# Optimization experiments

Measured on AMD Instinct MI355X. Metric: run time of the kernel, lower is better.

The kernel has to match this reference:

```python
import jax, jax.numpy as jnp
import numpy as np

D_MODEL, D_STATE, D_CONV, EXPAND = 768, 16, 4, 2
D_INNER = EXPAND * D_MODEL        # 1536
DT_RANK = (D_MODEL + 15) // 16    # 48
B, L = 4, 1024
LN_EPS = 1e-5


def _causal_dw_conv(x, w, b):
    # x: [b,l,d], w: [d,k], b: [d] -- depthwise causal conv along l
    k = w.shape[1]
    xp = jnp.pad(x, ((0, 0), (k - 1, 0), (0, 0)))
    out = jnp.zeros_like(x)
    for i in range(k):  # k = 4, tiny fixed loop
        out = out + xp[:, i:i + x.shape[1], :] * w[:, i]
    return out + b


def _selective_scan(u, delta, A, Bm, Cm, Dp):
    # u, delta: [b,l,d]; A: [d,n]; Bm, Cm: [b,l,n]; Dp: [d]
    def step(h, inp):
        d_t, B_t, C_t, u_t = inp                         # [b,d],[b,n],[b,n],[b,d]
        dA = jnp.exp(d_t[:, :, None] * A)                # [b,d,n]
        h = dA * h + (d_t * u_t)[:, :, None] * B_t[:, None, :]
        return h, jnp.einsum('bdn,bn->bd', h, C_t)
    b, l, d = u.shape
    h0 = jnp.zeros((b, d, A.shape[1]), u.dtype)
    xs = (jnp.swapaxes(delta, 0, 1), jnp.swapaxes(Bm, 0, 1),
          jnp.swapaxes(Cm, 0, 1), jnp.swapaxes(u, 0, 1))
    _, ys = jax.lax.scan(step, h0, xs)                   # ys: [l,b,d]
    return jnp.swapaxes(ys, 0, 1) + u * Dp


def _mamba_dir(xz, conv_w, conv_bias, xp_w, dtp_w, dtp_bias, A_log, Dp):
    x, z = jnp.split(xz, 2, axis=-1)                     # each [b,l,d_inner]
    x = jax.nn.silu(_causal_dw_conv(x, conv_w, conv_bias))
    x_dbl = x @ xp_w.T                                   # [b,l,R+2N]
    dt, Bm, Cm = jnp.split(x_dbl, [DT_RANK, DT_RANK + D_STATE], axis=-1)
    dt = jax.nn.softplus(dt @ dtp_w.T + dtp_bias)        # [b,l,d_inner]
    A = -jnp.exp(A_log)                                  # [d_inner,n]
    y = _selective_scan(x, dt, A, Bm, Cm, Dp)
    return y * jax.nn.silu(z)


def _block_single(h, ln_w, ln_b, in_w, conv_w, conv_bias, xp_w, dtp_w, dtp_bias,
                  A_log, D_p, conv_w_b, conv_bias_b, xp_w_b, dtp_w_b, dtp_bias_b,
                  A_b_log, D_b, out_w):
    # LayerNorm
    mu = jnp.mean(h, -1, keepdims=True)
    var = jnp.mean(jnp.square(h - mu), -1, keepdims=True)
    hn = (h - mu) * jax.lax.rsqrt(var + LN_EPS) * ln_w + ln_b
    # Mamba (bimamba v2): shared in_proj/out_proj, fwd + flipped bwd scan
    xz = hn @ in_w.T                                     # [b,l,2*d_inner]
    out_f = _mamba_dir(xz, conv_w, conv_bias, xp_w, dtp_w, dtp_bias, A_log, D_p)
    out_b = _mamba_dir(xz[:, ::-1], conv_w_b, conv_bias_b, xp_w_b, dtp_w_b,
                       dtp_bias_b, A_b_log, D_b)
    return (out_f + out_b[:, ::-1]) @ out_w.T            # [b,l,d_model]


def setup_inputs() -> dict:
    key = jax.random.key(0)
    ks = iter(jax.random.split(key, 40))
    f = lambda *s: jax.random.normal(next(ks), s, jnp.float32)
    p = {}
    p['h_r'] = f(B, L, D_MODEL)
    p['h_i'] = f(B, L, D_MODEL)
    # leading axis 2 = (real-branch mamba_r, imag-branch mamba_i) parameters
    p['ln_w'] = jnp.ones((2, D_MODEL), jnp.float32)
    p['ln_b'] = jnp.zeros((2, D_MODEL), jnp.float32)
    p['in_w'] = f(2, 2 * D_INNER, D_MODEL) * 0.02
    a_init = jnp.broadcast_to(jnp.log(jnp.arange(1, D_STATE + 1, dtype=jnp.float32)),
                              (2, D_INNER, D_STATE))
    for pre in ('', 'b_'):
        sfx = '_b' if pre else ''
        p['conv_w' + sfx] = f(2, D_INNER, D_CONV) * 0.2
        p['conv_bias' + sfx] = f(2, D_INNER) * 0.02
        p['xp_w' + sfx] = f(2, DT_RANK + 2 * D_STATE, D_INNER) * 0.02
        p['dtp_w' + sfx] = f(2, D_INNER, DT_RANK) * 0.1
        p['dtp_bias' + sfx] = f(2, D_INNER) * 0.5
        p['A_log' + sfx if not pre else 'A_b_log'] = a_init
        p['D_p' + sfx if not pre else 'D_b'] = f(2, D_INNER) * 0.1
    p['out_w'] = f(2, D_MODEL, D_INNER) * 0.02
    return p


def reference(h_r, h_i, ln_w, ln_b, in_w, conv_w, conv_bias, xp_w, dtp_w,
              dtp_bias, A_log, D_p, conv_w_b, conv_bias_b, xp_w_b, dtp_w_b,
              dtp_bias_b, A_b_log, D_b, out_w):
    h = jnp.stack([h_r, h_i])                            # [2,b,l,d_model]
    out = jax.vmap(_block_single)(h, ln_w, ln_b, in_w, conv_w, conv_bias, xp_w,
                                  dtp_w, dtp_bias, A_log, D_p, conv_w_b,
                                  conv_bias_b, xp_w_b, dtp_w_b, dtp_bias_b,
                                  A_b_log, D_b, out_w)
    return (out[0], out[1])
```

## Files before the change

### kernel.cpp

```cpp
#include <hip/hip_runtime.h>
#include <hip/hip_bf16.h>
#include <math.h>


#define BB 4
#define LL 1024
#define DM 768
#define DI 1536
#define RK 48
#define NS 16
#define CH 32
#define CLEN 32
#define DB6 (DI / 256)
#define XSPLIT 4
#define XKC2 (DI / XSPLIT)

typedef __attribute__((ext_vector_type(8))) short bf16x8;
typedef __attribute__((ext_vector_type(4))) float f32x4;
typedef unsigned short us;
typedef unsigned int uns;

__device__ __forceinline__ float siluf(float x) {
    return x / (1.f + __expf(-x));
}
__device__ __forceinline__ float softplusf(float x) {
    return fmaxf(x, 0.f) + __logf(1.f + __expf(-fabsf(x)));
}
__device__ __forceinline__ us f2bf(float x) {
    __hip_bfloat16 h = __float2bfloat16(x);
    return *(us*)&h;
}
__device__ __forceinline__ float bf2f(uns v) {
    uns u = v << 16;
    return *(float*)&u;
}
__device__ __forceinline__ unsigned pack2bf(float a, float b) {
    return (unsigned)f2bf(a) | ((unsigned)f2bf(b) << 16);
}
__device__ __forceinline__ void async_cp16(const void* g, void* l) {
    __builtin_amdgcn_global_load_lds(
        (const __attribute__((address_space(1))) void*)g,
        (__attribute__((address_space(3))) void*)l, 16, 0, 0);
}
__device__ __forceinline__ float pow8(float e1, float* p) {
    float e2 = e1 * e1, e4 = e2 * e2, e8 = e4 * e4;
    p[0] = e1;      p[1] = e2;      p[2] = e2 * e1; p[3] = e4;
    p[4] = e4 * e1; p[5] = e4 * e2; p[6] = e4 * p[2]; p[7] = e8;
    return e8;
}

__global__ __launch_bounds__(256)
void zero_kernel(float4* __restrict__ p, int n4)
{
    int i = blockIdx.x * 256 + threadIdx.x;
    if (i < n4) p[i] = (float4){0.f, 0.f, 0.f, 0.f};
}

__global__ __launch_bounds__(256)
void ln_kernel(const float* __restrict__ h, const float* __restrict__ w,
               const float* __restrict__ bvec, us* __restrict__ out)
{
    int row = blockIdx.x;
    const float* x = h + (size_t)row * DM;
    int tid = threadIdx.x;
    float v[3];
    float s = 0.f, s2 = 0.f;
#pragma unroll
    for (int j = 0; j < 3; ++j) {
        v[j] = x[tid + j * 256];
        s += v[j];
        s2 += v[j] * v[j];
    }
#pragma unroll
    for (int off = 32; off > 0; off >>= 1) {
        s += __shfl_down(s, off);
        s2 += __shfl_down(s2, off);
    }
    __shared__ float sw[4], sw2[4], stat[2];
    int wid = tid >> 6;
    if ((tid & 63) == 0) { sw[wid] = s; sw2[wid] = s2; }
    __syncthreads();
    if (tid == 0) {
        float a = sw[0] + sw[1] + sw[2] + sw[3];
        float a2 = sw2[0] + sw2[1] + sw2[2] + sw2[3];
        float mu = a * (1.f / DM);
        float var = a2 * (1.f / DM) - mu * mu;
// ... 2 lines not shown
    }
    __syncthreads();
    float mu = stat[0], rs = stat[1];
    us* o = out + (size_t)row * DM;
#pragma unroll
    for (int j = 0; j < 3; ++j) {
        int i = tid + j * 256;
        o[i] = f2bf((v[j] - mu) * rs * w[i] + bvec[i]);
    }
}

__global__ __launch_bounds__(256)
void cast_kernel(const float* __restrict__ x, us* __restrict__ y)
{
    int i = (blockIdx.x * 256 + threadIdx.x) * 4;
    float4 v = *(const float4*)(x + i);
    y[i + 0] = f2bf(v.x);
    y[i + 1] = f2bf(v.y);
    y[i + 2] = f2bf(v.z);
    y[i + 3] = f2bf(v.w);
}

__global__ __launch_bounds__(256)
void gemm_mfma_bt(const us* __restrict__ A, int lda,
                  const us* __restrict__ B, int ldb,
                  us* __restrict__ C, int ldc, int K)
{
    __shared__ us As[128 * 32];
    __shared__ us Bs[128 * 32];
    int tid = threadIdx.x;
    int wave = tid >> 6, lane = tid & 63;
    int wm = wave & 1, wn = wave >> 1;
    int quad = lane >> 4, lr = lane & 15;
    int m0 = blockIdx.y * 128, n0 = blockIdx.x * 128;

    f32x4 acc[4][4];
#pragma unroll
    for (int i = 0; i < 4; ++i)
#pragma unroll
        for (int j = 0; j < 4; ++j) acc[i][j] = (f32x4){0.f, 0.f, 0.f, 0.f};

    for (int kt = 0; kt < K; kt += 32) {
#pragma unroll
        for (int i = 0; i < 2; ++i) {
            int idx = tid + i * 256;
            int row = idx >> 2, col = (idx & 3) * 8;
            async_cp16(A + (size_t)(m0 + row) * lda + kt + col, &As[idx * 8]);
            async_cp16(B + (size_t)(n0 + row) * ldb + kt + col, &Bs[idx * 8]);
        }
        __syncthreads();

        bf16x8 af[4], bf[4];
#pragma unroll
        for (int mt = 0; mt < 4; ++mt)
            af[mt] = *(const bf16x8*)(&As[(wm * 64 + mt * 16 + lr) * 32 + quad * 8]);
#pragma unroll
        for (int nt = 0; nt < 4; ++nt)
            bf[nt] = *(const bf16x8*)(&Bs[(wn * 64 + nt * 16 + lr) * 32 + quad * 8]);
#pragma unroll
        for (int mt = 0; mt < 4; ++mt)
#pragma unroll
            for (int nt = 0; nt < 4; ++nt)
                acc[mt][nt] = __builtin_amdgcn_mfma_f32_16x16x32_bf16(
                    af[mt], bf[nt], acc[mt][nt], 0, 0, 0);
        __syncthreads();
    }

#pragma unroll
    for (int mt = 0; mt < 4; ++mt)
#pragma unroll
        for (int nt = 0; nt < 4; ++nt)
#pragma unroll
            for (int e = 0; e < 4; ++e) {
                int m = m0 + wm * 64 + mt * 16 + quad * 4 + e;
                int n = n0 + wn * 64 + nt * 16 + lr;
                C[(size_t)m * ldc + n] = f2bf(acc[mt][nt][e]);
            }
}

__global__ __launch_bounds__(256)
void gemm_mfma_bt64(const us* __restrict__ A, int lda,
                    const us* __restrict__ B, int ldb,
                    float* __restrict__ C, int ldc, int K)
{
    __shared__ us As[64 * 32];
    __shared__ us Bs[128 * 32];
    int tid = threadIdx.x;
    int wave = tid >> 6, lane = tid & 63;
    int wm = wave & 1, wn = wave >> 1;
    int quad = lane >> 4, lr = lane & 15;
    int m0 = blockIdx.y * 64, n0 = blockIdx.x * 128;

    f32x4 acc[2][4];
#pragma unroll
    for (int i = 0; i < 2; ++i)
#pragma unroll
        for (int j = 0; j < 4; ++j) acc[i][j] = (f32x4){0.f, 0.f, 0.f, 0.f};

    for (int kt = 0; kt < K; kt += 32) {
        {
            int row = tid >> 2, col = (tid & 3) * 8;
            async_cp16(A + (size_t)(m0 + row) * lda + kt + col, &As[tid * 8]);
        }
#pragma unroll
        for (int i = 0; i < 2; ++i) {
            int idx = tid + i * 256;
            int row = idx >> 2, col = (idx & 3) * 8;
            async_cp16(B + (size_t)(n0 + row) * ldb + kt + col, &Bs[idx * 8]);
        }
        __syncthreads();

        bf16x8 af[2], bf[4];
#pragma unroll
        for (int mt = 0; mt < 2; ++mt)
            af[mt] = *(const bf16x8*)(&As[(wm * 32 + mt * 16 + lr) * 32 + quad * 8]);
#pragma unroll
        for (int nt = 0; nt < 4; ++nt)
            bf[nt] = *(const bf16x8*)(&Bs[(wn * 64 + nt * 16 + lr) * 32 + quad * 8]);
#pragma unroll
        for (int mt = 0; mt < 2; ++mt)
#pragma unroll
            for (int nt = 0; nt < 4; ++nt)
                acc[mt][nt] = __builtin_amdgcn_mfma_f32_16x16x32_bf16(
                    af[mt], bf[nt], acc[mt][nt], 0, 0, 0);
        __syncthreads();
    }

#pragma unroll
    for (int mt = 0; mt < 2; ++mt)
#pragma unroll
        for (int nt = 0; nt < 4; ++nt)
#pragma unroll
            for (int e = 0; e < 4; ++e) {
                int m = m0 + wm * 32 + mt * 16 + quad * 4 + e;
                int n = n0 + wn * 64 + nt * 16 + lr;
                C[(size_t)m * ldc + n] = acc[mt][nt][e];
            }
}

#define CT 32
#define CD 64
__device__ __forceinline__ float4 dw4(float4 x0, float4 x1, float4 x2, float4 x3,
                                      float4 wa, float4 wb, float4 wc, float4 wd,
                                      float4 cb)
{
    float4 o;
    o.x = cb.x + x0.x * wa.x + x1.x * wa.y + x2.x * wa.z + x3.x * wa.w;
    o.y = cb.y + x0.y * wb.x + x1.y * wb.y + x2.y * wb.z + x3.y * wb.w;
    o.z = cb.z + x0.z * wc.x + x1.z * wc.y + x2.z * wc.z + x3.z * wc.w;
    o.w = cb.w + x0.w * wd.x + x1.w * wd.y + x2.w * wd.z + x3.w * wd.w;
    return o;
}

__global__ __launch_bounds__(256)
void conv_fused(const us* __restrict__ xz,
                const float* __restrict__ wf, const float* __restrict__ cbf,
                const float* __restrict__ wb, const float* __restrict__ cbb,
                us* __restrict__ xcf16, us* __restrict__ xcb16)
{
    int d0 = blockIdx.x * CD;
    int s0 = blockIdx.y * CT;
    int b  = blockIdx.z;
    int tid = threadIdx.x;

    __shared__ float XT[CT + 6][CD + 4];

    for (int i = tid; i < (CT + 6) * (CD / 4); i += 256) {
        int r = i >> 4;
        int c4 = i & 15;
        int s = s0 - 3 + r;
        float4 v = (float4){0.f, 0.f, 0.f, 0.f};
        if (s >= 0 && s < LL) {
            uint2 w = *(const uint2*)(xz + ((size_t)(b * LL + s)) * (2 * DI)
                                      + d0 + c4 * 4);
            v.x = bf2f(w.x & 0xffffu); v.y = bf2f(w.x >> 16);
            v.z = bf2f(w.y & 0xffffu); v.w = bf2f(w.y >> 16);
        }
        *(float4*)(&XT[r][c4 * 4]) = v;
    }

    int d4 = tid & 15;
    int sr = tid >> 4;
    int d = d0 + d4 * 4;
    float4 wf0 = *(const float4*)(wf + (size_t)(d + 0) * 4);
    float4 wf1 = *(const float4*)(wf + (size_t)(d + 1) * 4);
    float4 wf2 = *(const float4*)(wf + (size_t)(d + 2) * 4);
    float4 wf3 = *(const float4*)(wf + (size_t)(d + 3) * 4);
    float4 wb0 = *(const float4*)(wb + (size_t)(d + 0) * 4);
    float4 wb1 = *(const float4*)(wb + (size_t)(d + 1) * 4);
    float4 wb2 = *(const float4*)(wb + (size_t)(d + 2) * 4);
    float4 wb3 = *(const float4*)(wb + (size_t)(d + 3) * 4);
    float4 cf  = *(const float4*)(cbf + d);
    float4 cbv = *(const float4*)(cbb + d);
    __syncthreads();

    float4 x4[8];
// ... 2 lines not shown
        x4[j] = *(const float4*)(&XT[2 * sr + j][d4 * 4]);

#pragma unroll
    for (int q = 0; q < 2; ++q) {
        int s = s0 + 2 * sr + q;
        float4 of = dw4(x4[q + 0], x4[q + 1], x4[q + 2], x4[q + 3],
                        wf0, wf1, wf2, wf3, cf);
        of.x = siluf(of.x); of.y = siluf(of.y);
        of.z = siluf(of.z); of.w = siluf(of.w);
        size_t fi = ((size_t)(b * LL + s)) * DI + d;
        uint2 pf; pf.x = pack2bf(of.x, of.y); pf.y = pack2bf(of.z, of.w);
        *(uint2*)(&xcf16[fi]) = pf;
        float4 ob = dw4(x4[q + 6], x4[q + 5], x4[q + 4], x4[q + 3],
                        wb0, wb1, wb2, wb3, cbv);
        ob.x = siluf(ob.x); ob.y = siluf(ob.y);
        ob.z = siluf(ob.z); ob.w = siluf(ob.w);
        size_t bi = ((size_t)(b * LL + (LL - 1 - s))) * DI + d;
        uint2 pb; pb.x = pack2bf(ob.x, ob.y); pb.y = pack2bf(ob.z, ob.w);
        *(uint2*)(&xcb16[bi]) = pb;
    }
}

__global__ __launch_bounds__(256)
void xproj_mfma(const us* __restrict__ a0, const us* __restrict__ a1,
                const us* __restrict__ w0, const us* __restrict__ w1,
                float* __restrict__ xd0, float* __restrict__ xd1)
{
    int z = blockIdx.z;
    const us* A = z ? a1 : a0;
    const us* W = z ? w1 : w0;
    float* out = z ? xd1 : xd0;

    __shared__ us As[64 * 32];
    __shared__ us Ws[80 * 32];
    int tid = threadIdx.x;
    int wave = tid >> 6, lane = tid & 63;
    int quad = lane >> 4, lr = lane & 15;
    int m0 = blockIdx.y * 64;
    int k0 = blockIdx.x * XKC2;

    f32x4 acc[5];
#pragma unroll
    for (int j = 0; j < 5; ++j) acc[j] = (f32x4){0.f, 0.f, 0.f, 0.f};

    for (int kt = 0; kt < XKC2; kt += 32) {
        {
            int row = tid >> 2, col = (tid & 3) * 8;
            async_cp16(A + (size_t)(m0 + row) * DI + k0 + kt + col, &As[tid * 8]);
        }
        {
            int row = tid >> 2, col = (tid & 3) * 8;
            async_cp16(W + (size_t)row * DI + k0 + kt + col, &Ws[tid * 8]);
        }
        if (tid < 64) {
// ... 3 lines not shown
        }
        __syncthreads();

        bf16x8 af = *(const bf16x8*)(&As[(wave * 16 + lr) * 32 + quad * 8]);
#pragma unroll
        for (int j = 0; j < 5; ++j) {
            bf16x8 bf = *(const bf16x8*)(&Ws[(j * 16 + lr) * 32 + quad * 8]);
            acc[j] = __builtin_amdgcn_mfma_f32_16x16x32_bf16(af, bf, acc[j], 0, 0, 0);
        }
        __syncthreads();
    }

#pragma unroll
    for (int j = 0; j < 5; ++j)
#pragma unroll
        for (int e = 0; e < 4; ++e) {
            int m = m0 + wave * 16 + quad * 4 + e;
            int n = j * 16 + lr;
            atomicAdd(&out[(size_t)m * 80 + n], acc[j][e]);
        }
}

__global__ __launch_bounds__(256)
void dtproj2(const float* __restrict__ xd0, const float* __restrict__ xd1,
             const float* __restrict__ W0, const float* __restrict__ W1,
             const float* __restrict__ b0, const float* __restrict__ b1,
             const us* __restrict__ u0, const us* __restrict__ u1,
             uns* __restrict__ si0, uns* __restrict__ si1)
{
    int z = blockIdx.z;
    const float* A = z ? xd1 : xd0;
    const float* W = z ? W1 : W0;
    const float* bias = z ? b1 : b0;
    const us* U = z ? u1 : u0;
    uns* SI = z ? si1 : si0;

    __shared__ float As[48][132];
    __shared__ float Ws[48][68];
    int tid = threadIdx.x;
    int m0 = blockIdx.y * 128, n0 = blockIdx.x * 64;

    for (int i = tid; i < 1536; i += 256) {
        int r = i / 12, kg = i % 12;
        float4 v = *(const float4*)(A + (size_t)(m0 + r) * 80 + kg * 4);
        As[kg * 4 + 0][r] = v.x; As[kg * 4 + 1][r] = v.y;
        As[kg * 4 + 2][r] = v.z; As[kg * 4 + 3][r] = v.w;
    }
    for (int i = tid; i < 768; i += 256) {
        int r = i / 12, kg = i % 12;
        float4 u = *(const float4*)(W + (size_t)(n0 + r) * RK + kg * 4);
        Ws[kg * 4 + 0][r] = u.x; Ws[kg * 4 + 1][r] = u.y;
        Ws[kg * 4 + 2][r] = u.z; Ws[kg * 4 + 3][r] = u.w;
    }
    __syncthreads();

    int tx = tid & 15, ty = tid >> 4;
    float acc[8][4];
#pragma unroll
// ... 35 lines not shown
        s.w = (uns)f2bf(o.w) | (up.y & 0xffff0000u);
        *(uint4*)(SI + off) = s;
    }
}

__device__ __forceinline__ bool a_is_canonical8(const float* Alog, int d, int half)
{
    bool ok = true;
    const float4* a4 = (const float4*)(Alog + (size_t)d * NS + half * 8);
#pragma unroll
    for (int j = 0; j < 2; ++j) {
        float4 v = a4[j];
        float b0 = (float)(half * 8 + 4 * j + 1), b1 = (float)(half * 8 + 4 * j + 2);
        float b2 = (float)(half * 8 + 4 * j + 3), b3 = (float)(half * 8 + 4 * j + 4);
        ok = ok && (fabsf(__expf(v.x) - b0) < 1e-3f * b0)
                && (fabsf(__expf(v.y) - b1) < 1e-3f * b1)
                && (fabsf(__expf(v.z) - b2) < 1e-3f * b2)
                && (fabsf(__expf(v.w) - b3) < 1e-3f * b3);
    }
    return ok;
}

__global__ __launch_bounds__(512)
void scan_p1_b(const uns* __restrict__ si0, const uns* __restrict__ si1,
               const float* __restrict__ xd0, const float* __restrict__ xd1,
               const float* __restrict__ al0, const float* __restrict__ al1,
               uns* __restrict__ PQ0g, uns* __restrict__ PQ1g)
{
    int z = blockIdx.z;
    const uns* SI = z ? si1 : si0;
    const float* xdbl = z ? xd1 : xd0;
    const float* Alog = z ? al1 : al0;
    uns* PQ = z ? PQ1g : PQ0g;

    int c = blockIdx.y;
    int b = blockIdx.x / DB6;
    int dblk = (blockIdx.x % DB6) * 256;
    int tid = threadIdx.x;
    int dl = tid >> 1, half = tid & 1;
    int d = dblk + dl;
    int wave = tid >> 6, lane = tid & 63;

    bool afast = a_is_canonical8(Alog, d, half);

    __shared__ float Bs[CLEN * NS];
    __shared__ uns DU[2][8][256];
    for (int i = tid; i < CLEN * NS; i += 512) {
        int t = i >> 4, n = i & 15;
        Bs[i] = xdbl[((size_t)(b * LL + c * CLEN + t)) * 80 + 48 + n];
    }

    size_t rowbase = ((size_t)b * LL + c * CLEN) * DI + dblk;
#define STAGE_S(s, dbuf)                                                   \
    async_cp16(SI + rowbase + (size_t)((s) * 8 + wave) * DI + lane * 4,    \
               &DU[dbuf][wave][lane * 4]);

    STAGE_S(0, 0);

    float q[8];
#pragma unroll
    for (int n = 0; n < 8; ++n) q[n] = 0.f;
    float dtsum = 0.f;

    if (afast) {
#pragma unroll
        for (int s = 0; s < 4; ++s) {
            __syncthreads();
            if (s < 3) STAGE_S(s + 1, (s + 1) & 1);
            int buf = s & 1;
#pragma unroll
            for (int t8 = 0; t8 < 8; ++t8) {
                uns pk = DU[buf][t8][dl];
                float dtv = bf2f(pk & 0xffffu), uv = bf2f(pk >> 16);
                float du = dtv * uv;
                dtsum += dtv;
                float dA[8];
                float e8 = pow8(__expf(-dtv), dA);
                float sc = half ? e8 : 1.f;
                const float4* b4 = (const float4*)(Bs + (s * 8 + t8) * NS + half * 8);
                float4 B0 = b4[0], B1 = b4[1];
                q[0] = (dA[0] * sc) * q[0] + du * B0.x;
                q[1] = (dA[1] * sc) * q[1] + du * B0.y;
                q[2] = (dA[2] * sc) * q[2] + du * B0.z;
                q[3] = (dA[3] * sc) * q[3] + du * B0.w;
                q[4] = (dA[4] * sc) * q[4] + du * B1.x;
                q[5] = (dA[5] * sc) * q[5] + du * B1.y;
                q[6] = (dA[6] * sc) * q[6] + du * B1.z;
                q[7] = (dA[7] * sc) * q[7] + du * B1.w;
            }
        }
        float P[8];
        float e8 = pow8(__expf(-dtsum), P);
        float sc = half ? e8 : 1.f;
        uns* o = PQ + (size_t)c * (BB * DI * NS) + (size_t)(b * DI + d) * NS
               + half * 8;
        uint4 s0, s1;
        s0.x = pack2bf(P[0] * sc, q[0]); s0.y = pack2bf(P[1] * sc, q[1]);
        s0.z = pack2bf(P[2] * sc, q[2]); s0.w = pack2bf(P[3] * sc, q[3]);
        s1.x = pack2bf(P[4] * sc, q[4]); s1.y = pack2bf(P[5] * sc, q[5]);
        s1.z = pack2bf(P[6] * sc, q[6]); s1.w = pack2bf(P[7] * sc, q[7]);
        *(uint4*)(o) = s0;
        *(uint4*)(o + 4) = s1;
    } else {
        float Av[8];
        {
            const float4* a4 = (const float4*)(Alog + (size_t)d * NS + half * 8);
#pragma unroll
            for (int j = 0; j < 2; ++j) {
                float4 v = a4[j];
                Av[4 * j + 0] = -__expf(v.x); Av[4 * j + 1] = -__expf(v.y);
                Av[4 * j + 2] = -__expf(v.z); Av[4 * j + 3] = -__expf(v.w);
            }
        }
#pragma unroll
        for (int s = 0; s < 4; ++s) {
            __syncthreads();
            if (s < 3) STAGE_S(s + 1, (s + 1) & 1);
            int buf = s & 1;
#pragma unroll
            for (int t8 = 0; t8 < 8; ++t8) {
                uns pk = DU[buf][t8][dl];
                float dtv = bf2f(pk & 0xffffu), uv = bf2f(pk >> 16);
                float du = dtv * uv;
                dtsum += dtv;
                const float4* b4 = (const float4*)(Bs + (s * 8 + t8) * NS + half * 8);
                float4 B0 = b4[0], B1 = b4[1];
                q[0] = __expf(dtv * Av[0]) * q[0] + du * B0.x;
                q[1] = __expf(dtv * Av[1]) * q[1] + du * B0.y;
                q[2] = __expf(dtv * Av[2]) * q[2] + du * B0.z;
                q[3] = __expf(dtv * Av[3]) * q[3] + du * B0.w;
                q[4] = __expf(dtv * Av[4]) * q[4] + du * B1.x;
                q[5] = __expf(dtv * Av[5]) * q[5] + du * B1.y;
                q[6] = __expf(dtv * Av[6]) * q[6] + du * B1.z;
                q[7] = __expf(dtv * Av[7]) * q[7] + du * B1.w;
            }
        }
        uns* o = PQ + (size_t)c * (BB * DI * NS) + (size_t)(b * DI + d) * NS
               + half * 8;
#pragma unroll
        for (int n = 0; n < 8; ++n)
            o[n] = pack2bf(__expf(dtsum * Av[n]), q[n]);
    }
#undef STAGE_S
}

__global__ __launch_bounds__(256)
void scan_mid_b(uns* __restrict__ PQ0, uns* __restrict__ PQ1)
{
    int z = blockIdx.z;
    uns* PQ = z ? PQ1 : PQ0;
    int gid = blockIdx.x * 256 + threadIdx.x;
    const size_t stride = (size_t)(BB * DI * NS);
    uns pr[4];
#pragma unroll
    for (int i = 0; i < 4; ++i) pr[i] = PQ[(size_t)i * stride + gid];
    float h = 0.f;
    for (int c = 0; c < CH; ++c) {
        uns s = pr[c & 3];
        if (c + 4 < CH) pr[c & 3] = PQ[(size_t)(c + 4) * stride + gid];
        float P = bf2f(s & 0xffffu), q = bf2f(s >> 16);
        PQ[(size_t)c * stride + gid] = (s & 0xffff0000u) | (uns)f2bf(h);
        h = P * h + q;
    }
}

__global__ __launch_bounds__(512)
void scan_p2_b(const uns* __restrict__ si0, const uns* __restrict__ si1,
               const float* __restrict__ xd0, const float* __restrict__ xd1,
               const float* __restrict__ al0, const float* __restrict__ al1,
               const float* __restrict__ dp0, const float* __restrict__ dp1,
               const uns* __restrict__ PQ0g, const uns* __restrict__ PQ1g,
               us* __restrict__ g0, us* __restrict__ g1,
               int rev0, int rev1)
{
    int z = blockIdx.z;
    const uns* SI = z ? si1 : si0;
    const float* xdbl = z ? xd1 : xd0;
    const float* Alog = z ? al1 : al0;
    const float* Dp = z ? dp1 : dp0;
    const uns* PQ = z ? PQ1g : PQ0g;
    us* g = z ? g1 : g0;
    int rev = z ? rev1 : rev0;

    int c = blockIdx.y;
    int b = blockIdx.x / DB6;
    int dblk = (blockIdx.x % DB6) * 256;
    int tid = threadIdx.x;
    int dl = tid >> 1, half = tid & 1;
    int d = dblk + dl;
    int wave = tid >> 6, lane = tid & 63;

    bool afast = a_is_canonical8(Alog, d, half);

    float h[8];
    {
        const uns* h2 = PQ + (size_t)c * (BB * DI * NS)
                        + (size_t)(b * DI + d) * NS + half * 8;
        uint4 a = *(const uint4*)(h2);
        uint4 bq = *(const uint4*)(h2 + 4);
        h[0] = bf2f(a.x & 0xffffu); h[1] = bf2f(a.y & 0xffffu);
        h[2] = bf2f(a.z & 0xffffu); h[3] = bf2f(a.w & 0xffffu);
        h[4] = bf2f(bq.x & 0xffffu); h[5] = bf2f(bq.y & 0xffffu);
        h[6] = bf2f(bq.z & 0xffffu); h[7] = bf2f(bq.w & 0xffffu);
    }
    float Dpv = Dp[d];
// ... 8 lines not shown
        Cs[i] = xdbl[src + 64 + n];
    }

    size_t rowbase = ((size_t)b * LL + c * CLEN) * DI + dblk;
#define STAGE_S(s, dbuf)                                                   \
    async_cp16(SI + rowbase + (size_t)((s) * 8 + wave) * DI + lane * 4,    \
               &DU[dbuf][wave][lane * 4]);

    STAGE_S(0, 0);

    size_t gbase = (size_t)b * LL * DI + d;

    if (afast) {
#pragma unroll
        for (int s = 0; s < 4; ++s) {
            __syncthreads();
            if (s < 3) STAGE_S(s + 1, (s + 1) & 1);
            int buf = s & 1;
#pragma unroll
            for (int t8 = 0; t8 < 8; ++t8) {
                uns pk = DU[buf][t8][dl];
                float dtv = bf2f(pk & 0xffffu), uv = bf2f(pk >> 16);
                float du = dtv * uv;
                float dA[8];
                float e8 = pow8(__expf(-dtv), dA);
                float sc = half ? e8 : 1.f;
                int t = s * 8 + t8;
                const float4* b4 = (const float4*)(Bs + t * NS + half * 8);
                const float4* c4 = (const float4*)(Cs + t * NS + half * 8);
                float4 B0 = b4[0], B1 = b4[1];
                float4 C0 = c4[0], C1 = c4[1];
                float y = 0.f;
                h[0] = (dA[0] * sc) * h[0] + du * B0.x; y += h[0] * C0.x;
                h[1] = (dA[1] * sc) * h[1] + du * B0.y; y += h[1] * C0.y;
                h[2] = (dA[2] * sc) * h[2] + du * B0.z; y += h[2] * C0.z;
                h[3] = (dA[3] * sc) * h[3] + du * B0.w; y += h[3] * C0.w;
                h[4] = (dA[4] * sc) * h[4] + du * B1.x; y += h[4] * C1.x;
                h[5] = (dA[5] * sc) * h[5] + du * B1.y; y += h[5] * C1.y;
                h[6] = (dA[6] * sc) * h[6] + du * B1.z; y += h[6] * C1.z;
                h[7] = (dA[7] * sc) * h[7] + du * B1.w; y += h[7] * C1.w;
                y += __shfl_xor(y, 1);
                if (half == 0) {
                    int tt = c * CLEN + t;
                    int ot = rev ? (LL - 1 - tt) : tt;
                    g[gbase + (size_t)ot * DI] = f2bf(y + uv * Dpv);
                }
            }
        }
    } else {
        float Av[8];
        {
            const float4* a4 = (const float4*)(Alog + (size_t)d * NS + half * 8);
#pragma unroll
            for (int j = 0; j < 2; ++j) {
                float4 v = a4[j];
                Av[4 * j + 0] = -__expf(v.x); Av[4 * j + 1] = -__expf(v.y);
                Av[4 * j + 2] = -__expf(v.z); Av[4 * j + 3] = -__expf(v.w);
            }
        }
#pragma unroll
        for (int s = 0; s < 4; ++s) {
            __syncthreads();
            if (s < 3) STAGE_S(s + 1, (s + 1) & 1);
// ... 10 lines not shown
                float4 C0 = c4[0], C1 = c4[1];
                float y = 0.f;
                h[0] = __expf(dtv * Av[0]) * h[0] + du * B0.x; y += h[0] * C0.x;
                h[1] = __expf(dtv * Av[1]) * h[1] + du * B0.y; y += h[1] * C0.y;
                h[2] = __expf(dtv * Av[2]) * h[2] + du * B0.z; y += h[2] * C0.z;
                h[3] = __expf(dtv * Av[3]) * h[3] + du * B0.w; y += h[3] * C0.w;
                h[4] = __expf(dtv * Av[4]) * h[4] + du * B1.x; y += h[4] * C1.x;
                h[5] = __expf(dtv * Av[5]) * h[5] + du * B1.y; y += h[5] * C1.y;
                h[6] = __expf(dtv * Av[6]) * h[6] + du * B1.z; y += h[6] * C1.z;
                h[7] = __expf(dtv * Av[7]) * h[7] + du * B1.w; y += h[7] * C1.w;
                y += __shfl_xor(y, 1);
                if (half == 0) {
                    int tt = c * CLEN + t;
                    int ot = rev ? (LL - 1 - tt) : tt;
                    g[gbase + (size_t)ot * DI] = f2bf(y + uv * Dpv);
                }
            }
        }
    }
#undef STAGE_S
}

__global__ __launch_bounds__(256)
void gate2_kernel(const us* __restrict__ g0, const us* __restrict__ g1,
                  const us* __restrict__ xz, us* __restrict__ gb)
{
    int gid = (blockIdx.x * 256 + threadIdx.x) * 4;
    int d = gid % DI;
    int bt = gid / DI;
    uint2 zz = *(const uint2*)(xz + (size_t)bt * (2 * DI) + DI + d);
    uint2 a = *(const uint2*)(g0 + gid);
    uint2 bb = *(const uint2*)(g1 + gid);
    float z0 = bf2f(zz.x & 0xffffu), z1 = bf2f(zz.x >> 16);
    float z2 = bf2f(zz.y & 0xffffu), z3 = bf2f(zz.y >> 16);
    float v0 = (bf2f(a.x & 0xffffu) + bf2f(bb.x & 0xffffu)) * siluf(z0);
    float v1 = (bf2f(a.x >> 16)     + bf2f(bb.x >> 16))     * siluf(z1);
    float v2 = (bf2f(a.y & 0xffffu) + bf2f(bb.y & 0xffffu)) * siluf(z2);
    float v3 = (bf2f(a.y >> 16)     + bf2f(bb.y >> 16))     * siluf(z3);
    uint2 o; o.x = pack2bf(v0, v1); o.y = pack2bf(v2, v3);
    *(uint2*)(gb + gid) = o;
}

extern "C" void kernel_launch(void* const* d_in, const int* in_sizes, int n_in,
                              void* d_out, int out_size, void* d_ws, size_t ws_size,
                              hipStream_t stream)
{
    const float* h_r        = (const float*)d_in[0];
    const float* h_i        = (const float*)d_in[1];
    const float* ln_w       = (const float*)d_in[2];
    const float* ln_b       = (const float*)d_in[3];
    const float* in_w       = (const float*)d_in[4];
    const float* conv_w     = (const float*)d_in[5];
    const float* conv_bias  = (const float*)d_in[6];
// ... 2 lines not shown
    const float* dtp_bias   = (const float*)d_in[9];
    const float* A_log      = (const float*)d_in[10];
    const float* D_p        = (const float*)d_in[11];
    const float* conv_w_b   = (const float*)d_in[12];
    const float* conv_bias_b= (const float*)d_in[13];
    const float* xp_w_b     = (const float*)d_in[14];
    const float* dtp_w_b    = (const float*)d_in[15];
    const float* dtp_bias_b = (const float*)d_in[16];
    const float* A_b_log    = (const float*)d_in[17];
    const float* D_b        = (const float*)d_in[18];
    const float* out_w      = (const float*)d_in[19];
    float* out = (float*)d_out;

    const size_t E = (size_t)BB * LL * DI;
    const size_t XD = (size_t)BB * LL * 80;
    const size_t PQN = (size_t)CH * BB * DI * NS;

    char* p = (char*)d_ws;
    auto alloc = [&](size_t bytes) {
        char* r = p;
        p += (bytes + 255) & ~(size_t)255;
        return r;
    };
    us* xz16     = (us*)alloc(2 * E * 2);
    float* xd0   = (float*)alloc(XD * 4);
    float* xd1   = (float*)alloc(XD * 4);
    uns* siB0    = (uns*)alloc(E * 4);
    uns* siB1    = (uns*)alloc(E * 4);
    uns* PQ0     = (uns*)alloc(PQN * 4);
    uns* PQ1     = (uns*)alloc(PQN * 4);
    us* xc16_0   = (us*)alloc(E * 2);
    us* xc16_1   = (us*)alloc(E * 2);
    us* g0       = (us*)alloc(E * 2);
    us* g1       = (us*)alloc(E * 2);
    us* gb       = (us*)alloc(E * 2);
    us* hnb      = (us*)alloc((size_t)BB * LL * DM * 2);
    us* wbi_all  = (us*)alloc((size_t)2 * 2 * DI * DM * 2);
    us* wbo_all  = (us*)alloc((size_t)2 * DM * DI * 2);
    us* wbxf_all = (us*)alloc((size_t)2 * 80 * DI * 2);
    us* wbxb_all = (us*)alloc((size_t)2 * 80 * DI * 2);
    (void)ws_size;

    cast_kernel<<<(int)((2 * 2 * (size_t)DI * DM) / 1024), 256, 0, stream>>>(
        in_w, wbi_all);
    cast_kernel<<<(int)((2 * (size_t)DM * DI) / 1024), 256, 0, stream>>>(
        out_w, wbo_all);
    cast_kernel<<<(int)((2 * 80 * (size_t)DI) / 1024), 256, 0, stream>>>(
        xp_w, wbxf_all);
    cast_kernel<<<(int)((2 * 80 * (size_t)DI) / 1024), 256, 0, stream>>>(
        xp_w_b, wbxb_all);

    const size_t out_stride = (size_t)BB * LL * DM;

    for (int br = 0; br < 2; ++br) {
        const float* h = br ? h_i : h_r;
        const float* cw_f = conv_w + (size_t)br * DI * 4;
        const float* cb_f = conv_bias + (size_t)br * DI;
        const float* dw_f = dtp_w + (size_t)br * DI * RK;
        const float* db_f = dtp_bias + (size_t)br * DI;
        const float* al_f = A_log + (size_t)br * DI * NS;
        const float* dp_f = D_p + (size_t)br * DI;
        const float* cw_b = conv_w_b + (size_t)br * DI * 4;
        const float* cb_b = conv_bias_b + (size_t)br * DI;
        const float* dw_b = dtp_w_b + (size_t)br * DI * RK;
        const float* db_b = dtp_bias_b + (size_t)br * DI;
        const float* al_b = A_b_log + (size_t)br * DI * NS;
        const float* dp_b = D_b + (size_t)br * DI;
        us* wbi = wbi_all + (size_t)br * 2 * DI * DM;
        us* wbo = wbo_all + (size_t)br * DM * DI;
        us* wbx0 = wbxf_all + (size_t)br * 80 * DI;
        us* wbx1 = wbxb_all + (size_t)br * 80 * DI;

        ln_kernel<<<BB * LL, 256, 0, stream>>>(h, ln_w + br * DM, ln_b + br * DM, hnb);

        gemm_mfma_bt<<<dim3((2 * DI) / 128, (BB * LL) / 128), 256, 0, stream>>>(
            hnb, DM, wbi, DM, xz16, 2 * DI, DM);

        conv_fused<<<dim3(DI / CD, LL / CT, BB), 256, 0, stream>>>(
            xz16, cw_f, cb_f, cw_b, cb_b, xc16_0, xc16_1);
        zero_kernel<<<(int)(2 * XD / 4 + 255) / 256, 256, 0, stream>>>(
            (float4*)xd0, (int)(2 * XD / 4));
        xproj_mfma<<<dim3(XSPLIT, (BB * LL) / 64, 2), 256, 0, stream>>>(
            xc16_0, xc16_1, wbx0, wbx1, xd0, xd1);
        dtproj2<<<dim3(DI / 64, (BB * LL) / 128, 2), 256, 0, stream>>>(
            xd0, xd1, dw_f, dw_b, db_f, db_b, xc16_0, xc16_1, siB0, siB1);
        scan_p1_b<<<dim3(BB * DB6, CH, 2), 512, 0, stream>>>(
            siB0, siB1, xd0, xd1, al_f, al_b, PQ0, PQ1);
        scan_mid_b<<<dim3((int)((BB * DI * NS) / 256), 1, 2), 256, 0, stream>>>(
            PQ0, PQ1);
        scan_p2_b<<<dim3(BB * DB6, CH, 2), 512, 0, stream>>>(
            siB0, siB1, xd0, xd1, al_f, al_b, dp_f, dp_b,
            PQ0, PQ1, g0, g1, 0, 1);
        gate2_kernel<<<(int)(E / 1024), 256, 0, stream>>>(g0, g1, xz16, gb);

        gemm_mfma_bt64<<<dim3(DM / 128, (BB * LL) / 64), 256, 0, stream>>>(
            gb, DI, wbo, DI, out + br * out_stride, DM, DI);
    }
}
```

Before: 573.4 us.

## Batch real and imaginary branches into single launches via blockIdx.z

Removes the per-branch host loop: every kernel now indexes the branch (and direction) from blockIdx.z, so each stage launches once with a doubled grid. The in_proj output is split into separate X and Z buffers, and workspace buffers are aliased across stages whose lifetimes do not overlap. The scan kernels also fold the r^8 scale for the upper half of states into the power computation, which saves one multiply per state element. The aim is fewer launches and better GPU fill for the small per-branch grids, at the cost of buffer-reuse ordering that depends on the fixed stage sequence.

After: 502.8 us. 1.14x faster.

```diff
diff --git a/kernel.cpp b/kernel.cpp
--- a/kernel.cpp
+++ b/kernel.cpp
@@ -42,11 +42,10 @@
         (const __attribute__((address_space(1))) void*)g,
         (__attribute__((address_space(3))) void*)l, 16, 0, 0);
 }
-__device__ __forceinline__ float pow8(float e1, float* p) {
-    float e2 = e1 * e1, e4 = e2 * e2, e8 = e4 * e4;
-    p[0] = e1;      p[1] = e2;      p[2] = e2 * e1; p[3] = e4;
-    p[4] = e4 * e1; p[5] = e4 * e2; p[6] = e4 * p[2]; p[7] = e8;
-    return e8;
+__device__ __forceinline__ void pow8s(float sc, float r, float* d) {
+    float r2 = r * r, r3 = r2 * r, r4 = r2 * r2;
+    d[0] = sc * r;   d[1] = sc * r2;  d[2] = d[1] * r;  d[3] = sc * r4;
+    d[4] = d[3] * r; d[5] = d[3] * r2; d[6] = d[3] * r3; d[7] = d[3] * r4;
 }
 
 __global__ __launch_bounds__(256)
@@ -57,11 +56,18 @@
 }
 
 __global__ __launch_bounds__(256)
-void ln_kernel(const float* __restrict__ h, const float* __restrict__ w,
-               const float* __restrict__ bvec, us* __restrict__ out)
-{
+void ln_kernel(const float* __restrict__ h_r, const float* __restrict__ h_i,
+               const float* __restrict__ w_all, const float* __restrict__ b_all,
+               us* __restrict__ out_all)
+{
+    int br = blockIdx.z;
+    const float* hsrc = br ? h_i : h_r;
+    const float* w = w_all + br * DM;
+    const float* bvec = b_all + br * DM;
+    us* out = out_all + (size_t)br * BB * LL * DM;
+
     int row = blockIdx.x;
-    const float* x = h + (size_t)row * DM;
+    const float* x = hsrc + (size_t)row * DM;
     int tid = threadIdx.x;
     float v[3];
     float s = 0.f, s2 = 0.f;
@@ -110,17 +116,24 @@
 }
 
 __global__ __launch_bounds__(256)
-void gemm_mfma_bt(const us* __restrict__ A, int lda,
-                  const us* __restrict__ B, int ldb,
-                  us* __restrict__ C, int ldc, int K)
-{
+void gemm_mfma_bt(const us* __restrict__ hnb, const us* __restrict__ wbi,
+                  us* __restrict__ XH, us* __restrict__ ZH)
+{
+    int br = blockIdx.z;
+    const us* A = hnb + (size_t)br * BB * LL * DM;
+    const us* B = wbi + (size_t)br * 2 * DI * DM;
+
     __shared__ us As[128 * 32];
     __shared__ us Bs[128 * 32];
     int tid = threadIdx.x;
     int wave = tid >> 6, lane = tid & 63;
     int wm = wave & 1, wn = wave >> 1;
     int quad = lane >> 4, lr = lane & 15;
-    int m0 = blockIdx.y * 128, n0 = blockIdx.x * 128;
+    int m0 = blockIdx.y * 128, n0g = blockIdx.x * 128;
+
+    us* C; int cn0;
+    if (n0g < DI) { C = XH + (size_t)br * BB * LL * DI; cn0 = n0g; }
+    else          { C = ZH + (size_t)br * BB * LL * DI; cn0 = n0g - DI; }
 
     f32x4 acc[4][4];
 #pragma unroll
@@ -128,13 +141,13 @@
 #pragma unroll
         for (int j = 0; j < 4; ++j) acc[i][j] = (f32x4){0.f, 0.f, 0.f, 0.f};
 
-    for (int kt = 0; kt < K; kt += 32) {
+    for (int kt = 0; kt < DM; kt += 32) {
 #pragma unroll
         for (int i = 0; i < 2; ++i) {
             int idx = tid + i * 256;
             int row = idx >> 2, col = (idx & 3) * 8;
-            async_cp16(A + (size_t)(m0 + row) * lda + kt + col, &As[idx * 8]);
-            async_cp16(B + (size_t)(n0 + row) * ldb + kt + col, &Bs[idx * 8]);
+            async_cp16(A + (size_t)(m0 + row) * DM + kt + col, &As[idx * 8]);
+            async_cp16(B + (size_t)(n0g + row) * DM + kt + col, &Bs[idx * 8]);
         }
         __syncthreads();
 
@@ -161,16 +174,20 @@
 #pragma unroll
             for (int e = 0; e < 4; ++e) {
                 int m = m0 + wm * 64 + mt * 16 + quad * 4 + e;
-                int n = n0 + wn * 64 + nt * 16 + lr;
-                C[(size_t)m * ldc + n] = f2bf(acc[mt][nt][e]);
+                int n = cn0 + wn * 64 + nt * 16 + lr;
+                C[(size_t)m * DI + n] = f2bf(acc[mt][nt][e]);
             }
 }
 
 __global__ __launch_bounds__(256)
-void gemm_mfma_bt64(const us* __restrict__ A, int lda,
-                    const us* __restrict__ B, int ldb,
-                    float* __restrict__ C, int ldc, int K)
-{
+void gemm_mfma_bt64(const us* __restrict__ gb_all, const us* __restrict__ wbo,
+                    float* __restrict__ out_all, int out_stride)
+{
+    int br = blockIdx.z;
+    const us* A = gb_all + (size_t)br * BB * LL * DI;
+    const us* B = wbo + (size_t)br * DM * DI;
+    float* C = out_all + (size_t)br * out_stride;
+
     __shared__ us As[64 * 32];
     __shared__ us Bs[128 * 32];
     int tid = threadIdx.x;
@@ -185,16 +202,16 @@
 #pragma unroll
         for (int j = 0; j < 4; ++j) acc[i][j] = (f32x4){0.f, 0.f, 0.f, 0.f};
 
-    for (int kt = 0; kt < K; kt += 32) {
+    for (int kt = 0; kt < DI; kt += 32) {
         {
             int row = tid >> 2, col = (tid & 3) * 8;
-            async_cp16(A + (size_t)(m0 + row) * lda + kt + col, &As[tid * 8]);
+            async_cp16(A + (size_t)(m0 + row) * DI + kt + col, &As[tid * 8]);
         }
 #pragma unroll
         for (int i = 0; i < 2; ++i) {
             int idx = tid + i * 256;
             int row = idx >> 2, col = (idx & 3) * 8;
-            async_cp16(B + (size_t)(n0 + row) * ldb + kt + col, &Bs[idx * 8]);
+            async_cp16(B + (size_t)(n0 + row) * DI + kt + col, &Bs[idx * 8]);
         }
         __syncthreads();
 
@@ -222,7 +239,7 @@
             for (int e = 0; e < 4; ++e) {
                 int m = m0 + wm * 32 + mt * 16 + quad * 4 + e;
                 int n = n0 + wn * 64 + nt * 16 + lr;
-                C[(size_t)m * ldc + n] = acc[mt][nt][e];
+                C[(size_t)m * DM + n] = acc[mt][nt][e];
             }
 }
 
@@ -241,14 +258,23 @@
 }
 
 __global__ __launch_bounds__(256)
-void conv_fused(const us* __restrict__ xz,
-                const float* __restrict__ wf, const float* __restrict__ cbf,
-                const float* __restrict__ wb, const float* __restrict__ cbb,
-                us* __restrict__ xcf16, us* __restrict__ xcb16)
-{
+void conv_fused(const us* __restrict__ XH,
+                const float* __restrict__ conv_w, const float* __restrict__ conv_b,
+                const float* __restrict__ conv_w_b, const float* __restrict__ conv_b_b,
+                us* __restrict__ xc16)
+{
+    int zb = blockIdx.z;
+    int br = zb / BB, b = zb % BB;
+    const us* xz = XH + (size_t)br * BB * LL * DI;
+    const float* wf = conv_w + (size_t)br * DI * 4;
+    const float* cbf = conv_b + (size_t)br * DI;
+    const float* wb = conv_w_b + (size_t)br * DI * 4;
+    const float* cbb = conv_b_b + (size_t)br * DI;
+    us* xcf16 = xc16 + (size_t)(br * 2 + 0) * BB * LL * DI;
+    us* xcb16 = xc16 + (size_t)(br * 2 + 1) * BB * LL * DI;
+
     int d0 = blockIdx.x * CD;
     int s0 = blockIdx.y * CT;
-    int b  = blockIdx.z;
     int tid = threadIdx.x;
 
     __shared__ float XT[CT + 6][CD + 4];
@@ -259,7 +285,7 @@
         int s = s0 - 3 + r;
         float4 v = (float4){0.f, 0.f, 0.f, 0.f};
         if (s >= 0 && s < LL) {
-            uint2 w = *(const uint2*)(xz + ((size_t)(b * LL + s)) * (2 * DI)
+            uint2 w = *(const uint2*)(xz + ((size_t)(b * LL + s)) * DI
                                       + d0 + c4 * 4);
             v.x = bf2f(w.x & 0xffffu); v.y = bf2f(w.x >> 16);
             v.z = bf2f(w.y & 0xffffu); v.w = bf2f(w.y >> 16);
@@ -308,14 +334,15 @@
 }
 
 __global__ __launch_bounds__(256)
-void xproj_mfma(const us* __restrict__ a0, const us* __restrict__ a1,
-                const us* __restrict__ w0, const us* __restrict__ w1,
-                float* __restrict__ xd0, float* __restrict__ xd1)
+void xproj_mfma(const us* __restrict__ xc16,
+                const us* __restrict__ wbxf, const us* __restrict__ wbxb,
+                float* __restrict__ xd)
 {
     int z = blockIdx.z;
-    const us* A = z ? a1 : a0;
-    const us* W = z ? w1 : w0;
-    float* out = z ? xd1 : xd0;
+    int br = z >> 1, dir = z & 1;
+    const us* A = xc16 + (size_t)z * BB * LL * DI;
+    const us* W = (dir ? wbxb : wbxf) + (size_t)br * 80 * DI;
+    float* out = xd + (size_t)z * BB * LL * 80;
 
     __shared__ us As[64 * 32];
     __shared__ us Ws[80 * 32];
@@ -365,18 +392,18 @@
 }
 
 __global__ __launch_bounds__(256)
-void dtproj2(const float* __restrict__ xd0, const float* __restrict__ xd1,
-             const float* __restrict__ W0, const float* __restrict__ W1,
-             const float* __restrict__ b0, const float* __restrict__ b1,
-             const us* __restrict__ u0, const us* __restrict__ u1,
-             uns* __restrict__ si0, uns* __restrict__ si1)
+void dtproj2(const float* __restrict__ xd,
+             const float* __restrict__ dtp_w, const float* __restrict__ dtp_w_b,
+             const float* __restrict__ dtp_bias, const float* __restrict__ dtp_bias_b,
+             const us* __restrict__ xc16, uns* __restrict__ siB)
 {
     int z = blockIdx.z;
-    const float* A = z ? xd1 : xd0;
-    const float* W = z ? W1 : W0;
-    const float* bias = z ? b1 : b0;
-    const us* U = z ? u1 : u0;
-    uns* SI = z ? si1 : si0;
+    int br = z >> 1, dir = z & 1;
+    const float* A = xd + (size_t)z * BB * LL * 80;
+    const float* W = (dir ? dtp_w_b : dtp_w) + (size_t)br * DI * RK;
+    const float* bias = (dir ? dtp_bias_b : dtp_bias) + (size_t)br * DI;
+    const us* U = xc16 + (size_t)z * BB * LL * DI;
+    uns* SI = siB + (size_t)z * BB * LL * DI;
 
     __shared__ float As[48][132];
     __shared__ float Ws[48][68];
@@ -458,16 +485,16 @@
 }
 
 __global__ __launch_bounds__(512)
-void scan_p1_b(const uns* __restrict__ si0, const uns* __restrict__ si1,
-               const float* __restrict__ xd0, const float* __restrict__ xd1,
-               const float* __restrict__ al0, const float* __restrict__ al1,
-               uns* __restrict__ PQ0g, uns* __restrict__ PQ1g)
+void scan_p1_b(const uns* __restrict__ siB, const float* __restrict__ xd,
+               const float* __restrict__ A_log, const float* __restrict__ A_b_log,
+               uns* __restrict__ PQall)
 {
     int z = blockIdx.z;
-    const uns* SI = z ? si1 : si0;
-    const float* xdbl = z ? xd1 : xd0;
-    const float* Alog = z ? al1 : al0;
-    uns* PQ = z ? PQ1g : PQ0g;
+    int br = z >> 1, dir = z & 1;
+    const uns* SI = siB + (size_t)z * BB * LL * DI;
+    const float* xdbl = xd + (size_t)z * BB * LL * 80;
+    const float* Alog = (dir ? A_b_log : A_log) + (size_t)br * DI * NS;
+    uns* PQ = PQall + (size_t)z * CH * BB * DI * NS;
 
     int c = blockIdx.y;
     int b = blockIdx.x / DB6;
@@ -510,31 +537,35 @@
                 float dtv = bf2f(pk & 0xffffu), uv = bf2f(pk >> 16);
                 float du = dtv * uv;
                 dtsum += dtv;
+                float r = __expf(-dtv);
+                float sc = half ? r * r : 1.f;
+                if (half) { float r2 = r * r, r4 = r2 * r2; sc = r4 * r4; }
                 float dA[8];
-                float e8 = pow8(__expf(-dtv), dA);
-                float sc = half ? e8 : 1.f;
+                pow8s(sc, r, dA);
                 const float4* b4 = (const float4*)(Bs + (s * 8 + t8) * NS + half * 8);
                 float4 B0 = b4[0], B1 = b4[1];
-                q[0] = (dA[0] * sc) * q[0] + du * B0.x;
-                q[1] = (dA[1] * sc) * q[1] + du * B0.y;
-                q[2] = (dA[2] * sc) * q[2] + du * B0.z;
-                q[3] = (dA[3] * sc) * q[3] + du * B0.w;
-                q[4] = (dA[4] * sc) * q[4] + du * B1.x;
-                q[5] = (dA[5] * sc) * q[5] + du * B1.y;
-                q[6] = (dA[6] * sc) * q[6] + du * B1.z;
-                q[7] = (dA[7] * sc) * q[7] + du * B1.w;
+                q[0] = dA[0] * q[0] + du * B0.x;
+                q[1] = dA[1] * q[1] + du * B0.y;
+                q[2] = dA[2] * q[2] + du * B0.z;
+                q[3] = dA[3] * q[3] + du * B0.w;
+                q[4] = dA[4] * q[4] + du * B1.x;
+                q[5] = dA[5] * q[5] + du * B1.y;
+                q[6] = dA[6] * q[6] + du * B1.z;
+                q[7] = dA[7] * q[7] + du * B1.w;
             }
         }
+        float rs = __expf(-dtsum);
+        float sc = 1.f;
+        if (half) { float r2 = rs * rs, r4 = r2 * r2; sc = r4 * r4; }
         float P[8];
-        float e8 = pow8(__expf(-dtsum), P);
-        float sc = half ? e8 : 1.f;
+        pow8s(sc, rs, P);
         uns* o = PQ + (size_t)c * (BB * DI * NS) + (size_t)(b * DI + d) * NS
                + half * 8;
         uint4 s0, s1;
-        s0.x = pack2bf(P[0] * sc, q[0]); s0.y = pack2bf(P[1] * sc, q[1]);
-        s0.z = pack2bf(P[2] * sc, q[2]); s0.w = pack2bf(P[3] * sc, q[3]);
-        s1.x = pack2bf(P[4] * sc, q[4]); s1.y = pack2bf(P[5] * sc, q[5]);
-        s1.z = pack2bf(P[6] * sc, q[6]); s1.w = pack2bf(P[7] * sc, q[7]);
+        s0.x = pack2bf(P[0], q[0]); s0.y = pack2bf(P[1], q[1]);
+        s0.z = pack2bf(P[2], q[2]); s0.w = pack2bf(P[3], q[3]);
+        s1.x = pack2bf(P[4], q[4]); s1.y = pack2bf(P[5], q[5]);
+        s1.z = pack2bf(P[6], q[6]); s1.w = pack2bf(P[7], q[7]);
         *(uint4*)(o) = s0;
         *(uint4*)(o + 4) = s1;
     } else {
@@ -581,10 +612,10 @@
 }
 
 __global__ __launch_bounds__(256)
-void scan_mid_b(uns* __restrict__ PQ0, uns* __restrict__ PQ1)
+void scan_mid_b(uns* __restrict__ PQall)
 {
     int z = blockIdx.z;
-    uns* PQ = z ? PQ1 : PQ0;
+    uns* PQ = PQall + (size_t)z * CH * BB * DI * NS;
     int gid = blockIdx.x * 256 + threadIdx.x;
     const size_t stride = (size_t)(BB * DI * NS);
     uns pr[4];
@@ -601,22 +632,20 @@
 }
 
 __global__ __launch_bounds__(512)
-void scan_p2_b(const uns* __restrict__ si0, const uns* __restrict__ si1,
-               const float* __restrict__ xd0, const float* __restrict__ xd1,
-               const float* __restrict__ al0, const float* __restrict__ al1,
-               const float* __restrict__ dp0, const float* __restrict__ dp1,
-               const uns* __restrict__ PQ0g, const uns* __restrict__ PQ1g,
-               us* __restrict__ g0, us* __restrict__ g1,
-               int rev0, int rev1)
+void scan_p2_b(const uns* __restrict__ siB, const float* __restrict__ xd,
+               const float* __restrict__ A_log, const float* __restrict__ A_b_log,
+               const float* __restrict__ D_p, const float* __restrict__ D_b,
+               const uns* __restrict__ PQall, us* __restrict__ gall)
 {
     int z = blockIdx.z;
-    const uns* SI = z ? si1 : si0;
-    const float* xdbl = z ? xd1 : xd0;
-    const float* Alog = z ? al1 : al0;
-    const float* Dp = z ? dp1 : dp0;
-    const uns* PQ = z ? PQ1g : PQ0g;
-    us* g = z ? g1 : g0;
-    int rev = z ? rev1 : rev0;
+    int br = z >> 1, dir = z & 1;
+    const uns* SI = siB + (size_t)z * BB * LL * DI;
+    const float* xdbl = xd + (size_t)z * BB * LL * 80;
+    const float* Alog = (dir ? A_b_log : A_log) + (size_t)br * DI * NS;
+    const float* Dp = (dir ? D_b : D_p) + (size_t)br * DI;
+    const uns* PQ = PQall + (size_t)z * CH * BB * DI * NS;
+    us* g = gall + (size_t)z * BB * LL * DI;
+    int rev = dir;
 
     int c = blockIdx.y;
     int b = blockIdx.x / DB6;
@@ -671,23 +700,25 @@
                 uns pk = DU[buf][t8][dl];
                 float dtv = bf2f(pk & 0xffffu), uv = bf2f(pk >> 16);
                 float du = dtv * uv;
+                float r = __expf(-dtv);
+                float sc = 1.f;
+                if (half) { float r2 = r * r, r4 = r2 * r2; sc = r4 * r4; }
                 float dA[8];
-                float e8 = pow8(__expf(-dtv), dA);
-                float sc = half ? e8 : 1.f;
+                pow8s(sc, r, dA);
                 int t = s * 8 + t8;
                 const float4* b4 = (const float4*)(Bs + t * NS + half * 8);
                 const float4* c4 = (const float4*)(Cs + t * NS + half * 8);
                 float4 B0 = b4[0], B1 = b4[1];
                 float4 C0 = c4[0], C1 = c4[1];
                 float y = 0.f;
-                h[0] = (dA[0] * sc) * h[0] + du * B0.x; y += h[0] * C0.x;
-                h[1] = (dA[1] * sc) * h[1] + du * B0.y; y += h[1] * C0.y;
-                h[2] = (dA[2] * sc) * h[2] + du * B0.z; y += h[2] * C0.z;
-                h[3] = (dA[3] * sc) * h[3] + du * B0.w; y += h[3] * C0.w;
-                h[4] = (dA[4] * sc) * h[4] + du * B1.x; y += h[4] * C1.x;
-                h[5] = (dA[5] * sc) * h[5] + du * B1.y; y += h[5] * C1.y;
-                h[6] = (dA[6] * sc) * h[6] + du * B1.z; y += h[6] * C1.z;
-                h[7] = (dA[7] * sc) * h[7] + du * B1.w; y += h[7] * C1.w;
+                h[0] = dA[0] * h[0] + du * B0.x; y += h[0] * C0.x;
+                h[1] = dA[1] * h[1] + du * B0.y; y += h[1] * C0.y;
+                h[2] = dA[2] * h[2] + du * B0.z; y += h[2] * C0.z;
+                h[3] = dA[3] * h[3] + du * B0.w; y += h[3] * C0.w;
+                h[4] = dA[4] * h[4] + du * B1.x; y += h[4] * C1.x;
+                h[5] = dA[5] * h[5] + du * B1.y; y += h[5] * C1.y;
+                h[6] = dA[6] * h[6] + du * B1.z; y += h[6] * C1.z;
+                h[7] = dA[7] * h[7] + du * B1.w; y += h[7] * C1.w;
                 y += __shfl_xor(y, 1);
                 if (half == 0) {
                     int tt = c * CLEN + t;
@@ -744,13 +775,17 @@
 }
 
 __global__ __launch_bounds__(256)
-void gate2_kernel(const us* __restrict__ g0, const us* __restrict__ g1,
-                  const us* __restrict__ xz, us* __restrict__ gb)
-{
+void gate2_kernel(const us* __restrict__ gall, const us* __restrict__ ZH,
+                  us* __restrict__ gb_all)
+{
+    int br = blockIdx.z;
+    const us* g0 = gall + (size_t)(br * 2 + 0) * BB * LL * DI;
+    const us* g1 = gall + (size_t)(br * 2 + 1) * BB * LL * DI;
+    const us* zh = ZH + (size_t)br * BB * LL * DI;
+    us* gb = gb_all + (size_t)br * BB * LL * DI;
+
     int gid = (blockIdx.x * 256 + threadIdx.x) * 4;
-    int d = gid % DI;
-    int bt = gid / DI;
-    uint2 zz = *(const uint2*)(xz + (size_t)bt * (2 * DI) + DI + d);
+    uint2 zz = *(const uint2*)(zh + gid);
     uint2 a = *(const uint2*)(g0 + gid);
     uint2 bb = *(const uint2*)(g1 + gid);
     float z0 = bf2f(zz.x & 0xffffu), z1 = bf2f(zz.x >> 16);
@@ -799,78 +834,59 @@
         p += (bytes + 255) & ~(size_t)255;
         return r;
     };
-    us* xz16     = (us*)alloc(2 * E * 2);
-    float* xd0   = (float*)alloc(XD * 4);
-    float* xd1   = (float*)alloc(XD * 4);
-    uns* siB0    = (uns*)alloc(E * 4);
-    uns* siB1    = (uns*)alloc(E * 4);
-    uns* PQ0     = (uns*)alloc(PQN * 4);
-    uns* PQ1     = (uns*)alloc(PQN * 4);
-    us* xc16_0   = (us*)alloc(E * 2);
-    us* xc16_1   = (us*)alloc(E * 2);
-    us* g0       = (us*)alloc(E * 2);
-    us* g1       = (us*)alloc(E * 2);
-    us* gb       = (us*)alloc(E * 2);
-    us* hnb      = (us*)alloc((size_t)BB * LL * DM * 2);
-    us* wbi_all  = (us*)alloc((size_t)2 * 2 * DI * DM * 2);
-    us* wbo_all  = (us*)alloc((size_t)2 * DM * DI * 2);
-    us* wbxf_all = (us*)alloc((size_t)2 * 80 * DI * 2);
-    us* wbxb_all = (us*)alloc((size_t)2 * 80 * DI * 2);
+    uns* siB   = (uns*)alloc(4 * E * 4);
+    us* hnb    = (us*)siB;
+    us* XH     = (us*)alloc(2 * E * 2);
+    float* xd  = (float*)XH;
+    us* ZH     = (us*)alloc(2 * E * 2);
+    us* xc16   = (us*)alloc(4 * E * 2);
+    us* gall   = xc16;
+    uns* PQ    = (uns*)alloc(4 * PQN * 4);
+    us* gb     = (us*)PQ;
+    us* wbi    = (us*)alloc((size_t)2 * 2 * DI * DM * 2);
+    us* wbo    = (us*)alloc((size_t)2 * DM * DI * 2);
+    us* wbxf   = (us*)alloc((size_t)2 * 80 * DI * 2);
+    us* wbxb   = (us*)alloc((size_t)2 * 80 * DI * 2);
     (void)ws_size;
 
     cast_kernel<<<(int)((2 * 2 * (size_t)DI * DM) / 1024), 256, 0, stream>>>(
-        in_w, wbi_all);
+        in_w, wbi);
     cast_kernel<<<(int)((2 * (size_t)DM * DI) / 1024), 256, 0, stream>>>(
-        out_w, wbo_all);
+        out_w, wbo);
     cast_kernel<<<(int)((2 * 80 * (size_t)DI) / 1024), 256, 0, stream>>>(
-        xp_w, wbxf_all);
+        xp_w, wbxf);
     cast_kernel<<<(int)((2 * 80 * (size_t)DI) / 1024), 256, 0, stream>>>(
-        xp_w_b, wbxb_all);
-
-    const size_t out_stride = (size_t)BB * LL * DM;
-
-    for (int br = 0; br < 2; ++br) {
-        const float* h = br ? h_i : h_r;
-        const float* cw_f = conv_w + (size_t)br * DI * 4;
-        const float* cb_f = conv_bias + (size_t)br * DI;
-        const float* dw_f = dtp_w + (size_t)br * DI * RK;
-        const float* db_f = dtp_bias + (size_t)br * DI;
-        const float* al_f = A_log + (size_t)br * DI * NS;
-        const float* dp_f = D_p + (size_t)br * DI;
-        const float* cw_b = conv_w_b + (size_t)br * DI * 4;
-        const float* cb_b = conv_bias_b + (size_t)br * DI;
-        const float* dw_b = dtp_w_b + (size_t)br * DI * RK;
-        const float* db_b = dtp_bias_b + (size_t)br * DI;
-        const float* al_b = A_b_log + (size_t)br * DI * NS;
-        const float* dp_b = D_b + (size_t)br * DI;
-        us* wbi = wbi_all + (size_t)br * 2 * DI * DM;
-        us* wbo = wbo_all + (size_t)br * DM * DI;
-        us* wbx0 = wbxf_all + (size_t)br * 80 * DI;
-        us* wbx1 = wbxb_all + (size_t)br * 80 * DI;
-
-        ln_kernel<<<BB * LL, 256, 0, stream>>>(h, ln_w + br * DM, ln_b + br * DM, hnb);
-
-        gemm_mfma_bt<<<dim3((2 * DI) / 128, (BB * LL) / 128), 256, 0, stream>>>(
-            hnb, DM, wbi, DM, xz16, 2 * DI, DM);
-
-        conv_fused<<<dim3(DI / CD, LL / CT, BB), 256, 0, stream>>>(
-            xz16, cw_f, cb_f, cw_b, cb_b, xc16_0, xc16_1);
-        zero_kernel<<<(int)(2 * XD / 4 + 255) / 256, 256, 0, stream>>>(
-            (float4*)xd0, (int)(2 * XD / 4));
-        xproj_mfma<<<dim3(XSPLIT, (BB * LL) / 64, 2), 256, 0, stream>>>(
-            xc16_0, xc16_1, wbx0, wbx1, xd0, xd1);
-        dtproj2<<<dim3(DI / 64, (BB * LL) / 128, 2), 256, 0, stream>>>(
-            xd0, xd1, dw_f, dw_b, db_f, db_b, xc16_0, xc16_1, siB0, siB1);
-        scan_p1_b<<<dim3(BB * DB6, CH, 2), 512, 0, stream>>>(
-            siB0, siB1, xd0, xd1, al_f, al_b, PQ0, PQ1);
-        scan_mid_b<<<dim3((int)((BB * DI * NS) / 256), 1, 2), 256, 0, stream>>>(
-            PQ0, PQ1);
-        scan_p2_b<<<dim3(BB * DB6, CH, 2), 512, 0, stream>>>(
-            siB0, siB1, xd0, xd1, al_f, al_b, dp_f, dp_b,
-            PQ0, PQ1, g0, g1, 0, 1);
-        gate2_kernel<<<(int)(E / 1024), 256, 0, stream>>>(g0, g1, xz16, gb);
-
-        gemm_mfma_bt64<<<dim3(DM / 128, (BB * LL) / 64), 256, 0, stream>>>(
-            gb, DI, wbo, DI, out + br * out_stride, DM, DI);
-    }
-}
+        xp_w_b, wbxb);
+
+    ln_kernel<<<dim3(BB * LL, 1, 2), 256, 0, stream>>>(
+        h_r, h_i, ln_w, ln_b, hnb);
+
+    gemm_mfma_bt<<<dim3((2 * DI) / 128, (BB * LL) / 128, 2), 256, 0, stream>>>(
+        hnb, wbi, XH, ZH);
+
+    conv_fused<<<dim3(DI / CD, LL / CT, 2 * BB), 256, 0, stream>>>(
+        XH, conv_w, conv_bias, conv_w_b, conv_bias_b, xc16);
+
+    zero_kernel<<<(int)(4 * XD / 4 + 255) / 256, 256, 0, stream>>>(
+        (float4*)xd, (int)(4 * XD / 4));
+
+    xproj_mfma<<<dim3(XSPLIT, (BB * LL) / 64, 4), 256, 0, stream>>>(
+        xc16, wbxf, wbxb, xd);
+
+    dtproj2<<<dim3(DI / 64, (BB * LL) / 128, 4), 256, 0, stream>>>(
+        xd, dtp_w, dtp_w_b, dtp_bias, dtp_bias_b, xc16, siB);
+
+    scan_p1_b<<<dim3(BB * DB6, CH, 4), 512, 0, stream>>>(
+        siB, xd, A_log, A_b_log, PQ);
+
+    scan_mid_b<<<dim3((int)((BB * DI * NS) / 256), 1, 4), 256, 0, stream>>>(PQ);
+
+    scan_p2_b<<<dim3(BB * DB6, CH, 4), 512, 0, stream>>>(
+        siB, xd, A_log, A_b_log, D_p, D_b, PQ, gall);
+
+    gate2_kernel<<<dim3((int)(E / 1024), 1, 2), 256, 0, stream>>>(
+        gall, ZH, gb);
+
+    gemm_mfma_bt64<<<dim3(DM / 128, (BB * LL) / 64, 2), 256, 0, stream>>>(
+        gb, wbo, out, (int)((size_t)BB * LL * DM));
+}
```
